# Optimization experiments

Measured on AMD Instinct MI355X. Metric: run time of the kernel, lower is better.

The kernel has to match this reference:

```python
import jax, jax.numpy as jnp
import numpy as np

EPS = 1e-5
B, T, D, H = 4096, 256, 36, 64


def setup_inputs() -> dict:
    key = jax.random.key(0)
    ks = jax.random.split(key, 24)
    f32 = jnp.float32
    u = lambda k, shape, s: jax.random.uniform(k, shape, f32, -s, s)
    sH = 1.0 / np.sqrt(H)   # GRUCell / Linear(in=64) init scale
    sD = 1.0 / np.sqrt(D)
    sC = 1.0 / np.sqrt(2 * D)  # combine Linear(72,36)
    return {
        "values": jax.random.normal(ks[0], (B, T, D), f32),
        "masks": (jax.random.uniform(ks[1], (B, T, D)) > 0.2).astype(f32),
        "deltas": jax.random.uniform(ks[2], (B, T, D), f32) * 5.0,
        "label": (jax.random.uniform(ks[3], (B,)) > 0.5).astype(f32),
        "is_train": jnp.ones((B,), f32),
        # GRUCell(108, 64): gate order r, z, n (PyTorch convention)
        "W_ih": u(ks[4], (3 * H, 3 * D), sH),
        "W_hh": u(ks[5], (3 * H, H), sH),
        "b_ih": u(ks[6], (3 * H,), sH),
        "b_hh": u(ks[7], (3 * H,), sH),
        "hist_W": u(ks[8], (1, H), sH),
        "hist_b": u(ks[9], (1,), sH),
        "feat_W": u(ks[10], (D, D), sD),
        "feat_b": u(ks[11], (D,), sD),
        "decay_W": u(ks[12], (D, D), sD),
        "decay_b": u(ks[13], (D,), sD),
        "comb_W": u(ks[14], (D, 2 * D), sC),
        "comb_b": u(ks[15], (D,), sC),
        "out_W": u(ks[16], (1, H), sH),
        "out_b": u(ks[17], (1,), sH),
    }


def reference(values, masks, deltas, label, is_train,
              W_ih, W_hh, b_ih, b_hh, hist_W, hist_b,
              feat_W, feat_b, decay_W, decay_b,
              comb_W, comb_b, out_W, out_b):
    feat_Wm = feat_W * (1.0 - jnp.eye(D, dtype=feat_W.dtype))  # zero diagonal

    def step(carry, xs):
        h, h_sum, il = carry
        value, mask, delta = xs  # each [B, D]
        msum = jnp.sum(mask) + EPS
        value_x = h @ hist_W.T + hist_b                      # [B, 1], broadcasts
        il = il + jnp.sum(jnp.abs(value_x - value) * mask) / msum
        value_c = mask * value + (1.0 - mask) * value_x
        gamma = jnp.exp(-jax.nn.relu(delta @ decay_W.T + decay_b))
        beta = jax.nn.sigmoid(jnp.concatenate([gamma, mask], axis=1) @ comb_W.T + comb_b)
        value_z = value_c @ feat_Wm.T + feat_b
        il = il + jnp.sum(jnp.abs(value_z - value) * mask) / msum
        value_h = value_z * beta + value_x * (1.0 - beta)
        il = il + jnp.sum(jnp.abs(value_h - value) * mask) / msum
        value_c = mask * value + (1.0 - mask) * value_h
        x = jnp.concatenate([value_c, mask, gamma], axis=1)  # [B, 3D]
        gi = x @ W_ih.T + b_ih
        gh = h @ W_hh.T + b_hh
        i_r, i_z, i_n = jnp.split(gi, 3, axis=1)
        h_r, h_z, h_n = jnp.split(gh, 3, axis=1)
        r = jax.nn.sigmoid(i_r + h_r)
        z = jax.nn.sigmoid(i_z + h_z)
        n = jnp.tanh(i_n + r * h_n)
        h_new = (1.0 - z) * n + z * h
        return (h_new, h_sum + h_new, il), value_c

    init = (jnp.zeros((B, H), values.dtype),
            jnp.zeros((B, H), values.dtype),
            jnp.zeros((), values.dtype))
    xs = (values.transpose(1, 0, 2), masks.transpose(1, 0, 2), deltas.transpose(1, 0, 2))
    (h, h_sum, impute_loss), imp = jax.lax.scan(step, init, xs)

    impute_loss = impute_loss / T
    h_sum = h_sum / T
    logits = h_sum @ out_W.T + out_b                          # [B, 1]
    y = label.reshape(-1, 1)
    w = is_train.reshape(-1, 1)
    # binary_cross_entropy_with_logits, reduce=False
    bce = jnp.maximum(logits, 0.0) - logits * y + jnp.log1p(jnp.exp(-jnp.abs(logits)))
    class_loss = jnp.sum(bce * w) / (jnp.sum(w) + EPS)
    loss = class_loss + impute_loss  # alpha = 1.0
    pred = jax.nn.sigmoid(logits)
    impute_values = imp.transpose(1, 0, 2).reshape(B, T * D)  # concat over time on dim 1
    return loss, impute_values, pred
```

## Files before the change

### kernel.cpp

```cpp
#include <hip/hip_runtime.h>
#include <hip/hip_bf16.h>


#define Bsz 4096
#define Tn  256
#define Dn  36
#define ROWS 16
#define EPSf 1e-5f
#define VMST 38

using f32x4 = __attribute__((ext_vector_type(4))) float;
using s8    = __attribute__((ext_vector_type(8))) short;

__device__ __forceinline__ short f2bf(float x) {
  return (short)__bfloat16_as_ushort(__float2bfloat16(x));
}
__device__ __forceinline__ float sigf(float x) { return 1.f / (1.f + __expf(-x)); }
__device__ __forceinline__ float tanhfast(float x) { return 1.f - 2.f / (1.f + __expf(2.f * x)); }
__device__ __forceinline__ int fragoff(int row, int k) {
  return ((k >> 5) << 9) + (((k >> 3) & 3) << 7) + (row << 3) + (k & 7);
}
__device__ __forceinline__ float selq(f32x4 v, int s) {
  float a = (s & 1) ? v[1] : v[0];
  float b = (s & 1) ? v[3] : v[2];
  return (s & 2) ? b : a;
}

__global__ void msum_k(const float4* __restrict__ masks4, float* __restrict__ rmsum) {
  int t = blockIdx.x;
  float s = 0.f;
  for (int r = threadIdx.x; r < Bsz; r += 256) {
    const float4* mp = masks4 + ((size_t)r * Tn + t) * 9;
    #pragma unroll
    for (int j = 0; j < 9; ++j) { float4 v = mp[j]; s += v.x + v.y + v.z + v.w; }
  }
  __shared__ float red[256];
  red[threadIdx.x] = s;
  __syncthreads();
  for (int k = 128; k > 0; k >>= 1) {
    if (threadIdx.x < k) red[threadIdx.x] += red[threadIdx.x + k];
    __syncthreads();
  }
  if (threadIdx.x == 0) rmsum[t] = 1.f / (red[0] + EPSf);
}

__global__ __launch_bounds__(512) void brits_main(
    const float* __restrict__ values, const float* __restrict__ masks,
    const float* __restrict__ deltas, const float* __restrict__ label,
    const float* __restrict__ is_train,
    const float* __restrict__ W_ih, const float* __restrict__ W_hh,
    const float* __restrict__ b_ih, const float* __restrict__ b_hh,
    const float* __restrict__ hist_W, const float* __restrict__ hist_b,
    const float* __restrict__ feat_W, const float* __restrict__ feat_b,
    const float* __restrict__ decay_W, const float* __restrict__ decay_b,
    const float* __restrict__ comb_W, const float* __restrict__ comb_b,
    const float* __restrict__ out_W, const float* __restrict__ out_b,
    float* __restrict__ out, const float* __restrict__ rmsum,
    float* __restrict__ ws_acc ) {

  __shared__ __align__(16) float2 vm_s[2][ROWS * VMST];
  __shared__ float  red_s[512];
  __shared__ float  red16[16];
  __shared__ __align__(16) short hbuf[1024];
  __shared__ __align__(16) short dbuf[2][1024];
  __shared__ __align__(16) short xbuf[2][2048];
  __shared__ __align__(16) short vcbuf[4][1024];
  __shared__ __align__(16) short cxbuf[4][1536];

  const int tid  = threadIdx.x;
  const int w    = tid >> 6;
  const int lane = tid & 63;
  const int lc   = lane & 15;
  const int r4   = lane >> 4;
  const int row0 = blockIdx.x * ROWS;
  const int k0b  = r4 * 8;
  const int lw8  = lane * 8;

  const bool isG = (w < 4);
  const int  sW  = isG ? 0 : (w - 4);
  const int  dim = 16 * (isG ? w : 0) + lc;
  const int  myrow = 4 * r4 + sW;

  s8 bf[23];
  #pragma unroll
  for (int i = 0; i < 23; ++i) bf[i] = (s8)(short)0;

  if (isG) {
    #pragma unroll
    for (int g = 0; g < 3; ++g) {
      const int n = 64 * g + dim;
      #pragma unroll
      for (int kt = 0; kt < 4; ++kt) {
        s8 f;
        #pragma unroll
        for (int e = 0; e < 8; ++e) {
          int xk = k0b + 32 * kt + e;
          float wv = 0.f;
          if (xk < 72) wv = W_ih[n * 108 + 36 + xk];
          else if (xk < 108) wv = W_ih[n * 108 + xk - 72];
          f[e] = f2bf(wv);
        }
        bf[g * 4 + kt] = f;
      }
      #pragma unroll
      for (int kt = 0; kt < 2; ++kt) {
        s8 f;
        #pragma unroll
        for (int e = 0; e < 8; ++e) f[e] = f2bf(W_hh[n * 64 + k0b + 32 * kt + e]);
        bf[12 + g * 2 + kt] = f;
      }
    }
  } else {
    #pragma unroll
    for (int t3 = 0; t3 < 3; ++t3) {
      const int col = 16 * t3 + lc;
      const bool cok = (col < Dn);
      #pragma unroll
      for (int kt = 0; kt < 2; ++kt) {
        s8 fd, ff;
        #pragma unroll
        for (int e = 0; e < 8; ++e) {
          int k = k0b + 32 * kt + e;
          fd[e] = f2bf((cok && k < Dn) ? decay_W[col * Dn + k] : 0.f);
          ff[e] = f2bf((cok && k < Dn && k != col) ? feat_W[col * Dn + k] : 0.f);
        }
        bf[t3 * 2 + kt] = fd;
        bf[6 + t3 * 2 + kt] = ff;
      }
      #pragma unroll
      for (int kt = 0; kt < 3; ++kt) {
        s8 f;
        #pragma unroll
        for (int e = 0; e < 8; ++e) {
          int k = k0b + 32 * kt + e;
          f[e] = f2bf((cok && k < 72) ? comb_W[col * 72 + k] : 0.f);
        }
        bf[12 + t3 * 3 + kt] = f;
      }
    }
    #pragma unroll
    for (int kt = 0; kt < 2; ++kt) {
      s8 f;
      #pragma unroll
      for (int e = 0; e < 8; ++e) f[e] = f2bf(hist_W[k0b + 32 * kt + e]);
      bf[21 + kt] = f;
    }
  }

  float db3[3] = {0,0,0}, fb3[3] = {0,0,0}, cb3[3] = {0,0,0};
  float br = 0.f, bz = 0.f, bin_ = 0.f, bhn = 0.f, ow = 0.f;
  if (isG) {
    br   = b_ih[dim] + b_hh[dim];
    bz   = b_ih[64 + dim] + b_hh[64 + dim];
    bin_ = b_ih[128 + dim];
    bhn  = b_hh[128 + dim];
    ow   = out_W[dim];
  } else {
    #pragma unroll
    for (int t3 = 0; t3 < 3; ++t3) {
      int col = 16 * t3 + lc;
      if (col < Dn) { db3[t3] = decay_b[col]; fb3[t3] = feat_b[col]; cb3[t3] = comb_b[col]; }
    }
  }
  const float histb = hist_b[0];
  const int hb = fragoff(0, dim);

  const bool stg = (tid < 144);
  const int srow = tid / 9;
  const int squad = tid - srow * 9;
  const size_t sbase = ((size_t)(row0 + srow) * Tn) * Dn + squad * 4;
  const int sfo = fragoff(srow, squad * 4);
  const int svo = srow * VMST + squad * 4;

  const int mrow = 4 * (lane / 9) + sW;
  const int mc0  = (lane % 9) * 4;

  for (int i = tid; i < 1024; i += 512) {
    hbuf[i] = 0; dbuf[0][i] = 0; dbuf[1][i] = 0;
    vcbuf[0][i] = 0; vcbuf[1][i] = 0; vcbuf[2][i] = 0; vcbuf[3][i] = 0;
  }
  for (int i = tid; i < 2048; i += 512) { xbuf[0][i] = 0; xbuf[1][i] = 0; }
  for (int i = tid; i < 1536; i += 512) {
    cxbuf[0][i] = 0; cxbuf[1][i] = 0; cxbuf[2][i] = 0; cxbuf[3][i] = 0;
  }
  __syncthreads();

  float4 pv = {0,0,0,0}, pm = {0,0,0,0}, pd = {0,0,0,0};
  if (stg) {
    float4 v0 = *(const float4*)&values[sbase];
    float4 m0 = *(const float4*)&masks[sbase];
    float4 d0 = *(const float4*)&deltas[sbase];
    *(float4*)&vm_s[0][svo]     = make_float4(v0.x, m0.x, v0.y, m0.y);
    *(float4*)&vm_s[0][svo + 2] = make_float4(v0.z, m0.z, v0.w, m0.w);
    union { short s[4]; uint2 u; } td, tm;
    td.s[0]=f2bf(d0.x); td.s[1]=f2bf(d0.y); td.s[2]=f2bf(d0.z); td.s[3]=f2bf(d0.w);
    tm.s[0]=f2bf(m0.x); tm.s[1]=f2bf(m0.y); tm.s[2]=f2bf(m0.z); tm.s[3]=f2bf(m0.w);
    *(uint2*)&dbuf[0][sfo] = td.u;
    *(uint2*)&xbuf[0][sfo] = tm.u;
    pv = *(const float4*)&values[sbase + Dn];
    pm = *(const float4*)&masks[sbase + Dn];
    pd = *(const float4*)&deltas[sbase + Dn];
  }
  __syncthreads();
  if (!isG && lane < 36) {
    #pragma unroll
    for (int j = 0; j < 4; ++j)
      cxbuf[sW][fragoff(mrow, 36 + mc0 + j)] = f2bf(vm_s[0][mrow * VMST + mc0 + j].y);
  }

  float hreg[4] = {0.f, 0.f, 0.f, 0.f};
  float lacc[4] = {0.f, 0.f, 0.f, 0.f};
  float il = 0.f;
  __syncthreads();

  #pragma unroll 1
  for (int t = 0; t < Tn; ++t) {
    const float srm = rmsum[t];
    const int p = t & 1;
    f32x4 A0 = {0,0,0,0}, A1 = {0,0,0,0}, A2 = {0,0,0,0}, A3 = {0,0,0,0};

    if (isG) {
      s8 ah0 = *(const s8*)&hbuf[lw8];
      s8 ah1 = *(const s8*)&hbuf[512 + lw8];
      s8 ax0 = *(const s8*)&xbuf[p][lw8];
      A0 = __builtin_amdgcn_mfma_f32_16x16x32_bf16(ah0, bf[12], A0, 0, 0, 0);
      A0 = __builtin_amdgcn_mfma_f32_16x16x32_bf16(ah1, bf[13], A0, 0, 0, 0);
      A1 = __builtin_amdgcn_mfma_f32_16x16x32_bf16(ah0, bf[14], A1, 0, 0, 0);
      A1 = __builtin_amdgcn_mfma_f32_16x16x32_bf16(ah1, bf[15], A1, 0, 0, 0);
      A3 = __builtin_amdgcn_mfma_f32_16x16x32_bf16(ah0, bf[16], A3, 0, 0, 0);
      A3 = __builtin_amdgcn_mfma_f32_16x16x32_bf16(ah1, bf[17], A3, 0, 0, 0);
      A0 = __builtin_amdgcn_mfma_f32_16x16x32_bf16(ax0, bf[0], A0, 0, 0, 0);
      A1 = __builtin_amdgcn_mfma_f32_16x16x32_bf16(ax0, bf[4], A1, 0, 0, 0);
      A2 = __builtin_amdgcn_mfma_f32_16x16x32_bf16(ax0, bf[8], A2, 0, 0, 0);
      if (stg && t + 1 < Tn) {
        *(float4*)&vm_s[p ^ 1][svo]     = make_float4(pv.x, pm.x, pv.y, pm.y);
        *(float4*)&vm_s[p ^ 1][svo + 2] = make_float4(pv.z, pm.z, pv.w, pm.w);
        union { short s[4]; uint2 u; } td, tm;
        td.s[0]=f2bf(pd.x); td.s[1]=f2bf(pd.y); td.s[2]=f2bf(pd.z); td.s[3]=f2bf(pd.w);
        tm.s[0]=f2bf(pm.x); tm.s[1]=f2bf(pm.y); tm.s[2]=f2bf(pm.z); tm.s[3]=f2bf(pm.w);
        *(uint2*)&dbuf[p ^ 1][sfo] = td.u;
        *(uint2*)&xbuf[p ^ 1][sfo] = tm.u;
      }
      if (stg && t + 2 < Tn) {
        size_t o = sbase + (size_t)(t + 2) * Dn;
        pv = *(const float4*)&values[o];
        pm = *(const float4*)&masks[o];
        pd = *(const float4*)&deltas[o];
      }
    } else {
      s8 ah0 = *(const s8*)&hbuf[lw8];
      s8 ah1 = *(const s8*)&hbuf[512 + lw8];
      s8 ad0 = *(const s8*)&dbuf[p][lw8];
      s8 ad1 = *(const s8*)&dbuf[p][512 + lw8];
      f32x4 X = {0,0,0,0};
      X = __builtin_amdgcn_mfma_f32_16x16x32_bf16(ah0, bf[21], X, 0, 0, 0);
      X = __builtin_amdgcn_mfma_f32_16x16x32_bf16(ah1, bf[22], X, 0, 0, 0);
      f32x4 Gm0 = {0,0,0,0}, Gm1 = {0,0,0,0}, Gm2 = {0,0,0,0};
      Gm0 = __builtin_amdgcn_mfma_f32_16x16x32_bf16(ad0, bf[0], Gm0, 0, 0, 0);
      Gm0 = __builtin_amdgcn_mfma_f32_16x16x32_bf16(ad1, bf[1], Gm0, 0, 0, 0);
      Gm1 = __builtin_amdgcn_mfma_f32_16x16x32_bf16(ad0, bf[2], Gm1, 0, 0, 0);
      Gm1 = __builtin_amdgcn_mfma_f32_16x16x32_bf16(ad1, bf[3], Gm1, 0, 0, 0);
      Gm2 = __builtin_amdgcn_mfma_f32_16x16x32_bf16(ad0, bf[4], Gm2, 0, 0, 0);
      Gm2 = __builtin_amdgcn_mfma_f32_16x16x32_bf16(ad1, bf[5], Gm2, 0, 0, 0);
      const float vx = selq(X, sW) + histb;

      float v3[3], m3[3];
      #pragma unroll
      for (int t3 = 0; t3 < 3; ++t3) {
        const int col = 16 * t3 + lc;
        float gmv = (t3 == 0) ? selq(Gm0, sW) : (t3 == 1) ? selq(Gm1, sW) : selq(Gm2, sW);
        v3[t3] = 0.f; m3[t3] = 0.f;
        if (col < Dn) {
          float g = __expf(-fmaxf(gmv + db3[t3], 0.f));
          short gbv = f2bf(g);
          xbuf[p][fragoff(myrow, 36 + col)] = gbv;
          cxbuf[sW][fragoff(myrow, col)]    = gbv;
          float2 vm = vm_s[p][myrow * VMST + col];
          v3[t3] = vm.x; m3[t3] = vm.y;
          il += srm * fabsf(vx - vm.x) * vm.y;
          vcbuf[sW][fragoff(myrow, col)] = f2bf(vm.y * vm.x + (1.f - vm.y) * vx);
        }
      }
      s8 av0 = *(const s8*)&vcbuf[sW][lw8];
      s8 av1 = *(const s8*)&vcbuf[sW][512 + lw8];
      f32x4 Z0 = {0,0,0,0}, Z1 = {0,0,0,0}, Z2 = {0,0,0,0};
      Z0 = __builtin_amdgcn_mfma_f32_16x16x32_bf16(av0, bf[6],  Z0, 0, 0, 0);
      Z0 = __builtin_amdgcn_mfma_f32_16x16x32_bf16(av1, bf[7],  Z0, 0, 0, 0);
      Z1 = __builtin_amdgcn_mfma_f32_16x16x32_bf16(av0, bf[8],  Z1, 0, 0, 0);
      Z1 = __builtin_amdgcn_mfma_f32_16x16x32_bf16(av1, bf[9],  Z1, 0, 0, 0);
      Z2 = __builtin_amdgcn_mfma_f32_16x16x32_bf16(av0, bf[10], Z2, 0, 0, 0);
      Z2 = __builtin_amdgcn_mfma_f32_16x16x32_bf16(av1, bf[11], Z2, 0, 0, 0);
      s8 ac0 = *(const s8*)&cxbuf[sW][lw8];
      s8 ac1 = *(const s8*)&cxbuf[sW][512 + lw8];
      s8 ac2 = *(const s8*)&cxbuf[sW][1024 + lw8];
      f32x4 B0 = {0,0,0,0}, B1 = {0,0,0,0}, B2 = {0,0,0,0};
      B0 = __builtin_amdgcn_mfma_f32_16x16x32_bf16(ac0, bf[12], B0, 0, 0, 0);
      B0 = __builtin_amdgcn_mfma_f32_16x16x32_bf16(ac1, bf[13], B0, 0, 0, 0);
      B0 = __builtin_amdgcn_mfma_f32_16x16x32_bf16(ac2, bf[14], B0, 0, 0, 0);
      B1 = __builtin_amdgcn_mfma_f32_16x16x32_bf16(ac0, bf[15], B1, 0, 0, 0);
      B1 = __builtin_amdgcn_mfma_f32_16x16x32_bf16(ac1, bf[16], B1, 0, 0, 0);
      B1 = __builtin_amdgcn_mfma_f32_16x16x32_bf16(ac2, bf[17], B1, 0, 0, 0);
      B2 = __builtin_amdgcn_mfma_f32_16x16x32_bf16(ac0, bf[18], B2, 0, 0, 0);
      B2 = __builtin_amdgcn_mfma_f32_16x16x32_bf16(ac1, bf[19], B2, 0, 0, 0);
      B2 = __builtin_amdgcn_mfma_f32_16x16x32_bf16(ac2, bf[20], B2, 0, 0, 0);
      #pragma unroll
      for (int t3 = 0; t3 < 3; ++t3) {
        const int col = 16 * t3 + lc;
        if (col < Dn) {
          float zv = (t3 == 0) ? selq(Z0, sW) : (t3 == 1) ? selq(Z1, sW) : selq(Z2, sW);
          float bv = (t3 == 0) ? selq(B0, sW) : (t3 == 1) ? selq(B1, sW) : selq(B2, sW);
          float beta = sigf(bv + cb3[t3]);
          float vz = zv + fb3[t3];
          il += srm * fabsf(vz - v3[t3]) * m3[t3];
          float vh = vz * beta + vx * (1.f - beta);
          il += srm * fabsf(vh - v3[t3]) * m3[t3];
          float vc2 = m3[t3] * v3[t3] + (1.f - m3[t3]) * vh;
          out[1 + ((size_t)(row0 + myrow) * Tn + t) * Dn + col] = vc2;
          xbuf[p][fragoff(myrow, 72 + col)] = f2bf(vc2);
        }
      }
    }
    __syncthreads();

    if (isG) {
      s8 ax1 = *(const s8*)&xbuf[p][512 + lw8];
      s8 ax2 = *(const s8*)&xbuf[p][1024 + lw8];
      s8 ax3 = *(const s8*)&xbuf[p][1536 + lw8];
      A0 = __builtin_amdgcn_mfma_f32_16x16x32_bf16(ax1, bf[1], A0, 0, 0, 0);
      A1 = __builtin_amdgcn_mfma_f32_16x16x32_bf16(ax1, bf[5], A1, 0, 0, 0);
      A2 = __builtin_amdgcn_mfma_f32_16x16x32_bf16(ax1, bf[9], A2, 0, 0, 0);
      A0 = __builtin_amdgcn_mfma_f32_16x16x32_bf16(ax2, bf[2], A0, 0, 0, 0);
      A1 = __builtin_amdgcn_mfma_f32_16x16x32_bf16(ax2, bf[6], A1, 0, 0, 0);
      A2 = __builtin_amdgcn_mfma_f32_16x16x32_bf16(ax2, bf[10], A2, 0, 0, 0);
      A0 = __builtin_amdgcn_mfma_f32_16x16x32_bf16(ax3, bf[3], A0, 0, 0, 0);
      A1 = __builtin_amdgcn_mfma_f32_16x16x32_bf16(ax3, bf[7], A1, 0, 0, 0);
      A2 = __builtin_amdgcn_mfma_f32_16x16x32_bf16(ax3, bf[11], A2, 0, 0, 0);
      #pragma unroll
      for (int q = 0; q < 4; ++q) {
        float rg = sigf(A0[q] + br);
        float zg = sigf(A1[q] + bz);
        float ng = tanhfast(A2[q] + bin_ + rg * (A3[q] + bhn));
        float hn = (1.f - zg) * ng + zg * hreg[q];
        hreg[q] = hn;
        lacc[q] += hn * ow;
        hbuf[hb + (r4 * 4 + q) * 8] = f2bf(hn);
      }
    } else {
      if (t + 1 < Tn && lane < 36) {
        #pragma unroll
        for (int j = 0; j < 4; ++j)
          cxbuf[sW][fragoff(mrow, 36 + mc0 + j)] =
              f2bf(vm_s[p ^ 1][mrow * VMST + mc0 + j].y);
      }
    }
    __syncthreads();
  }

  red_s[tid] = il;
  __syncthreads();
  for (int k = 256; k > 0; k >>= 1) {
    if (tid < k) red_s[tid] += red_s[tid + k];
    __syncthreads();
  }
  if (tid == 0) atomicAdd(&ws_acc[0], red_s[0]);
  if (tid < 16) red16[tid] = 0.f;
  __syncthreads();
  if (isG) {
    #pragma unroll
    for (int q = 0; q < 4; ++q) atomicAdd(&red16[r4 * 4 + q], lacc[q]);
  }
  __syncthreads();

  if (tid < ROWS) {
    float lg = red16[tid] / (float)Tn + out_b[0];
    int rg = row0 + tid;
    float pred = sigf(lg);
    out[1 + (size_t)Bsz * Tn * Dn + rg] = pred;
    float y = label[rg], wt = is_train[rg];
    float bce = fmaxf(lg, 0.f) - lg * y + log1pf(__expf(-fabsf(lg)));
    atomicAdd(&ws_acc[1], bce * wt);
    atomicAdd(&ws_acc[2], wt);
  }
}

__global__ void fin_k(const float* __restrict__ ws, float* __restrict__ out) {
  out[0] = ws[1] / (ws[2] + EPSf) + ws[0] / (float)Tn;
}

extern "C" void kernel_launch(void* const* d_in, const int* in_sizes, int n_in,
                              void* d_out, int out_size, void* d_ws, size_t ws_size,
                              hipStream_t stream) {
  const float* values   = (const float*)d_in[0];
  const float* masks    = (const float*)d_in[1];
  const float* deltas   = (const float*)d_in[2];
  const float* label    = (const float*)d_in[3];
  const float* is_train = (const float*)d_in[4];
  const float* W_ih     = (const float*)d_in[5];
  const float* W_hh     = (const float*)d_in[6];
  const float* b_ih     = (const float*)d_in[7];
  const float* b_hh     = (const float*)d_in[8];
  const float* hist_W   = (const float*)d_in[9];
  const float* hist_b   = (const float*)d_in[10];
  const float* feat_W   = (const float*)d_in[11];
  const float* feat_b   = (const float*)d_in[12];
  const float* decay_W  = (const float*)d_in[13];
  const float* decay_b  = (const float*)d_in[14];
  const float* comb_W   = (const float*)d_in[15];
  const float* comb_b   = (const float*)d_in[16];
  const float* out_W    = (const float*)d_in[17];
  const float* out_b    = (const float*)d_in[18];

  float* ws = (float*)d_ws;
  float* rmsum = ws + 4;
  float* out = (float*)d_out;

  hipMemsetAsync(d_ws, 0, 16, stream);
  msum_k<<<Tn, 256, 0, stream>>>((const float4*)masks, rmsum);
  brits_main<<<Bsz / ROWS, 512, 0, stream>>>(
      values, masks, deltas, label, is_train, W_ih, W_hh, b_ih, b_hh,
      hist_W, hist_b, feat_W, feat_b, decay_W, decay_b, comb_W, comb_b,
      out_W, out_b, out, rmsum, ws);
  fin_k<<<1, 1, 0, stream>>>(ws, out);
}
```

Measured before the change: 447.6 us.

## Precompute next-step decay/beta in phase two and move weights to LDS

The decay (gamma) and combine (beta) matmuls for step t+1 move into the second phase of step t, which was mostly idle for the side waves. This shortens the critical first phase that gates the GRU update. W_hh and comb_W fragments now live in shared memory rather than registers, cutting register use so launch_bounds(512,4) can be requested. The cost is more LDS traffic and a larger LDS footprint, which may itself limit occupancy.

```diff
diff --git a/kernel.cpp b/kernel.cpp
--- a/kernel.cpp
+++ b/kernel.cpp
@@ -25,6 +25,7 @@
   float b = (s & 1) ? v[3] : v[2];
   return (s & 2) ? b : a;
 }
+#define MFMA __builtin_amdgcn_mfma_f32_16x16x32_bf16
 
 __global__ void msum_k(const float4* __restrict__ masks4, float* __restrict__ rmsum) {
   int t = blockIdx.x;
@@ -44,7 +45,7 @@
   if (threadIdx.x == 0) rmsum[t] = 1.f / (red[0] + EPSf);
 }
 
-__global__ __launch_bounds__(512) void brits_main(
+__global__ __launch_bounds__(512, 4) void brits_main(
     const float* __restrict__ values, const float* __restrict__ masks,
     const float* __restrict__ deltas, const float* __restrict__ label,
     const float* __restrict__ is_train,
@@ -59,13 +60,14 @@
     float* __restrict__ ws_acc ) {
 
   __shared__ __align__(16) float2 vm_s[2][ROWS * VMST];
-  __shared__ float  red_s[512];
-  __shared__ float  red16[16];
   __shared__ __align__(16) short hbuf[1024];
   __shared__ __align__(16) short dbuf[2][1024];
   __shared__ __align__(16) short xbuf[2][2048];
   __shared__ __align__(16) short vcbuf[4][1024];
   __shared__ __align__(16) short cxbuf[4][1536];
+  __shared__ __align__(16) short whh_l[24 * 512];
+  __shared__ __align__(16) short comb_l[9 * 512];
+  __shared__ float red16[16];
 
   const int tid  = threadIdx.x;
   const int w    = tid >> 6;
@@ -81,9 +83,9 @@
   const int  dim = 16 * (isG ? w : 0) + lc;
   const int  myrow = 4 * r4 + sW;
 
-  s8 bf[23];
+  s8 bf[14];
   #pragma unroll
-  for (int i = 0; i < 23; ++i) bf[i] = (s8)(short)0;
+  for (int i = 0; i < 14; ++i) bf[i] = (s8)(short)0;
 
   if (isG) {
     #pragma unroll
@@ -107,7 +109,7 @@
         s8 f;
         #pragma unroll
         for (int e = 0; e < 8; ++e) f[e] = f2bf(W_hh[n * 64 + k0b + 32 * kt + e]);
-        bf[12 + g * 2 + kt] = f;
+        *(s8*)&whh_l[(w * 6 + g * 2 + kt) * 512 + lw8] = f;
       }
     }
   } else {
@@ -127,23 +129,30 @@
         bf[t3 * 2 + kt] = fd;
         bf[6 + t3 * 2 + kt] = ff;
       }
-      #pragma unroll
-      for (int kt = 0; kt < 3; ++kt) {
-        s8 f;
-        #pragma unroll
-        for (int e = 0; e < 8; ++e) {
-          int k = k0b + 32 * kt + e;
-          f[e] = f2bf((cok && k < 72) ? comb_W[col * 72 + k] : 0.f);
-        }
-        bf[12 + t3 * 3 + kt] = f;
-      }
     }
     #pragma unroll
     for (int kt = 0; kt < 2; ++kt) {
       s8 f;
       #pragma unroll
       for (int e = 0; e < 8; ++e) f[e] = f2bf(hist_W[k0b + 32 * kt + e]);
-      bf[21 + kt] = f;
+      bf[12 + kt] = f;
+    }
+    if (w == 4) {
+      #pragma unroll
+      for (int t3 = 0; t3 < 3; ++t3) {
+        const int col = 16 * t3 + lc;
+        const bool cok = (col < Dn);
+        #pragma unroll
+        for (int kt = 0; kt < 3; ++kt) {
+          s8 f;
+          #pragma unroll
+          for (int e = 0; e < 8; ++e) {
+            int k = k0b + 32 * kt + e;
+            f[e] = f2bf((cok && k < 72) ? comb_W[col * 72 + k] : 0.f);
+          }
+          *(s8*)&comb_l[(t3 * 3 + kt) * 512 + lw8] = f;
+        }
+      }
     }
   }
 
@@ -202,10 +211,46 @@
     pd = *(const float4*)&deltas[sbase + Dn];
   }
   __syncthreads();
-  if (!isG && lane < 36) {
-    #pragma unroll
-    for (int j = 0; j < 4; ++j)
-      cxbuf[sW][fragoff(mrow, 36 + mc0 + j)] = f2bf(vm_s[0][mrow * VMST + mc0 + j].y);
+
+  float bq[3] = {0.f, 0.f, 0.f};
+  if (!isG) {
+    s8 ad0 = *(const s8*)&dbuf[0][lw8];
+    s8 ad1 = *(const s8*)&dbuf[0][512 + lw8];
+    f32x4 G0 = {0,0,0,0}, G1 = {0,0,0,0}, G2 = {0,0,0,0};
+    G0 = MFMA(ad0, bf[0], G0, 0,0,0); G0 = MFMA(ad1, bf[1], G0, 0,0,0);
+    G1 = MFMA(ad0, bf[2], G1, 0,0,0); G1 = MFMA(ad1, bf[3], G1, 0,0,0);
+    G2 = MFMA(ad0, bf[4], G2, 0,0,0); G2 = MFMA(ad1, bf[5], G2, 0,0,0);
+    #pragma unroll
+    for (int t3 = 0; t3 < 3; ++t3) {
+      int col = 16 * t3 + lc;
+      if (col < Dn) {
+        float gm = (t3==0) ? selq(G0,sW) : (t3==1) ? selq(G1,sW) : selq(G2,sW);
+        short gbv = f2bf(__expf(-fmaxf(gm + db3[t3], 0.f)));
+        xbuf[0][fragoff(myrow, 36 + col)] = gbv;
+        cxbuf[sW][fragoff(myrow, col)] = gbv;
+      }
+    }
+    if (lane < 36) {
+      #pragma unroll
+      for (int j = 0; j < 4; ++j)
+        cxbuf[sW][fragoff(mrow, 36 + mc0 + j)] = f2bf(vm_s[0][mrow * VMST + mc0 + j].y);
+    }
+    s8 ac0 = *(const s8*)&cxbuf[sW][lw8];
+    s8 ac1 = *(const s8*)&cxbuf[sW][512 + lw8];
+    s8 ac2 = *(const s8*)&cxbuf[sW][1024 + lw8];
+    f32x4 B0 = {0,0,0,0}, B1 = {0,0,0,0}, B2 = {0,0,0,0};
+    B0 = MFMA(ac0, *(const s8*)&comb_l[0*512+lw8], B0, 0,0,0);
+    B0 = MFMA(ac1, *(const s8*)&comb_l[1*512+lw8], B0, 0,0,0);
+    B0 = MFMA(ac2, *(const s8*)&comb_l[2*512+lw8], B0, 0,0,0);
+    B1 = MFMA(ac0, *(const s8*)&comb_l[3*512+lw8], B1, 0,0,0);
+    B1 = MFMA(ac1, *(const s8*)&comb_l[4*512+lw8], B1, 0,0,0);
+    B1 = MFMA(ac2, *(const s8*)&comb_l[5*512+lw8], B1, 0,0,0);
+    B2 = MFMA(ac0, *(const s8*)&comb_l[6*512+lw8], B2, 0,0,0);
+    B2 = MFMA(ac1, *(const s8*)&comb_l[7*512+lw8], B2, 0,0,0);
+    B2 = MFMA(ac2, *(const s8*)&comb_l[8*512+lw8], B2, 0,0,0);
+    bq[0] = sigf(selq(B0,sW) + cb3[0]);
+    bq[1] = sigf(selq(B1,sW) + cb3[1]);
+    bq[2] = sigf(selq(B2,sW) + cb3[2]);
   }
 
   float hreg[4] = {0.f, 0.f, 0.f, 0.f};
@@ -220,18 +265,20 @@
     f32x4 A0 = {0,0,0,0}, A1 = {0,0,0,0}, A2 = {0,0,0,0}, A3 = {0,0,0,0};
 
     if (isG) {
+      const int wb = w * 6 * 512;
       s8 ah0 = *(const s8*)&hbuf[lw8];
       s8 ah1 = *(const s8*)&hbuf[512 + lw8];
+      A0 = MFMA(ah0, *(const s8*)&whh_l[wb + lw8],        A0, 0,0,0);
+      A0 = MFMA(ah1, *(const s8*)&whh_l[wb + 512 + lw8],  A0, 0,0,0);
+      A1 = MFMA(ah0, *(const s8*)&whh_l[wb + 1024 + lw8], A1, 0,0,0);
+      A1 = MFMA(ah1, *(const s8*)&whh_l[wb + 1536 + lw8], A1, 0,0,0);
+      A3 = MFMA(ah0, *(const s8*)&whh_l[wb + 2048 + lw8], A3, 0,0,0);
+      A3 = MFMA(ah1, *(const s8*)&whh_l[wb + 2560 + lw8], A3, 0,0,0);
       s8 ax0 = *(const s8*)&xbuf[p][lw8];
-      A0 = __builtin_amdgcn_mfma_f32_16x16x32_bf16(ah0, bf[12], A0, 0, 0, 0);
-      A0 = __builtin_amdgcn_mfma_f32_16x16x32_bf16(ah1, bf[13], A0, 0, 0, 0);
-      A1 = __builtin_amdgcn_mfma_f32_16x16x32_bf16(ah0, bf[14], A1, 0, 0, 0);
-      A1 = __builtin_amdgcn_mfma_f32_16x16x32_bf16(ah1, bf[15], A1, 0, 0, 0);
-      A3 = __builtin_amdgcn_mfma_f32_16x16x32_bf16(ah0, bf[16], A3, 0, 0, 0);
-      A3 = __builtin_amdgcn_mfma_f32_16x16x32_bf16(ah1, bf[17], A3, 0, 0, 0);
-      A0 = __builtin_amdgcn_mfma_f32_16x16x32_bf16(ax0, bf[0], A0, 0, 0, 0);
-      A1 = __builtin_amdgcn_mfma_f32_16x16x32_bf16(ax0, bf[4], A1, 0, 0, 0);
-      A2 = __builtin_amdgcn_mfma_f32_16x16x32_bf16(ax0, bf[8], A2, 0, 0, 0);
+      s8 ax1 = *(const s8*)&xbuf[p][512 + lw8];
+      A0 = MFMA(ax0, bf[0], A0, 0,0,0); A0 = MFMA(ax1, bf[1], A0, 0,0,0);
+      A1 = MFMA(ax0, bf[4], A1, 0,0,0); A1 = MFMA(ax1, bf[5], A1, 0,0,0);
+      A2 = MFMA(ax0, bf[8], A2, 0,0,0); A2 = MFMA(ax1, bf[9], A2, 0,0,0);
       if (stg && t + 1 < Tn) {
         *(float4*)&vm_s[p ^ 1][svo]     = make_float4(pv.x, pm.x, pv.y, pm.y);
         *(float4*)&vm_s[p ^ 1][svo + 2] = make_float4(pv.z, pm.z, pv.w, pm.w);
@@ -250,31 +297,16 @@
     } else {
       s8 ah0 = *(const s8*)&hbuf[lw8];
       s8 ah1 = *(const s8*)&hbuf[512 + lw8];
-      s8 ad0 = *(const s8*)&dbuf[p][lw8];
-      s8 ad1 = *(const s8*)&dbuf[p][512 + lw8];
       f32x4 X = {0,0,0,0};
-      X = __builtin_amdgcn_mfma_f32_16x16x32_bf16(ah0, bf[21], X, 0, 0, 0);
-      X = __builtin_amdgcn_mfma_f32_16x16x32_bf16(ah1, bf[22], X, 0, 0, 0);
-      f32x4 Gm0 = {0,0,0,0}, Gm1 = {0,0,0,0}, Gm2 = {0,0,0,0};
-      Gm0 = __builtin_amdgcn_mfma_f32_16x16x32_bf16(ad0, bf[0], Gm0, 0, 0, 0);
-      Gm0 = __builtin_amdgcn_mfma_f32_16x16x32_bf16(ad1, bf[1], Gm0, 0, 0, 0);
-      Gm1 = __builtin_amdgcn_mfma_f32_16x16x32_bf16(ad0, bf[2], Gm1, 0, 0, 0);
-      Gm1 = __builtin_amdgcn_mfma_f32_16x16x32_bf16(ad1, bf[3], Gm1, 0, 0, 0);
-      Gm2 = __builtin_amdgcn_mfma_f32_16x16x32_bf16(ad0, bf[4], Gm2, 0, 0, 0);
-      Gm2 = __builtin_amdgcn_mfma_f32_16x16x32_bf16(ad1, bf[5], Gm2, 0, 0, 0);
+      X = MFMA(ah0, bf[12], X, 0,0,0);
+      X = MFMA(ah1, bf[13], X, 0,0,0);
       const float vx = selq(X, sW) + histb;
-
       float v3[3], m3[3];
       #pragma unroll
       for (int t3 = 0; t3 < 3; ++t3) {
-        const int col = 16 * t3 + lc;
-        float gmv = (t3 == 0) ? selq(Gm0, sW) : (t3 == 1) ? selq(Gm1, sW) : selq(Gm2, sW);
+        int col = 16 * t3 + lc;
         v3[t3] = 0.f; m3[t3] = 0.f;
         if (col < Dn) {
-          float g = __expf(-fmaxf(gmv + db3[t3], 0.f));
-          short gbv = f2bf(g);
-          xbuf[p][fragoff(myrow, 36 + col)] = gbv;
-          cxbuf[sW][fragoff(myrow, col)]    = gbv;
           float2 vm = vm_s[p][myrow * VMST + col];
           v3[t3] = vm.x; m3[t3] = vm.y;
           il += srm * fabsf(vx - vm.x) * vm.y;
@@ -284,35 +316,16 @@
       s8 av0 = *(const s8*)&vcbuf[sW][lw8];
       s8 av1 = *(const s8*)&vcbuf[sW][512 + lw8];
       f32x4 Z0 = {0,0,0,0}, Z1 = {0,0,0,0}, Z2 = {0,0,0,0};
-      Z0 = __builtin_amdgcn_mfma_f32_16x16x32_bf16(av0, bf[6],  Z0, 0, 0, 0);
-      Z0 = __builtin_amdgcn_mfma_f32_16x16x32_bf16(av1, bf[7],  Z0, 0, 0, 0);
-      Z1 = __builtin_amdgcn_mfma_f32_16x16x32_bf16(av0, bf[8],  Z1, 0, 0, 0);
-      Z1 = __builtin_amdgcn_mfma_f32_16x16x32_bf16(av1, bf[9],  Z1, 0, 0, 0);
-      Z2 = __builtin_amdgcn_mfma_f32_16x16x32_bf16(av0, bf[10], Z2, 0, 0, 0);
-      Z2 = __builtin_amdgcn_mfma_f32_16x16x32_bf16(av1, bf[11], Z2, 0, 0, 0);
-      s8 ac0 = *(const s8*)&cxbuf[sW][lw8];
-      s8 ac1 = *(const s8*)&cxbuf[sW][512 + lw8];
-      s8 ac2 = *(const s8*)&cxbuf[sW][1024 + lw8];
-      f32x4 B0 = {0,0,0,0}, B1 = {0,0,0,0}, B2 = {0,0,0,0};
-      B0 = __builtin_amdgcn_mfma_f32_16x16x32_bf16(ac0, bf[12], B0, 0, 0, 0);
-      B0 = __builtin_amdgcn_mfma_f32_16x16x32_bf16(ac1, bf[13], B0, 0, 0, 0);
-      B0 = __builtin_amdgcn_mfma_f32_16x16x32_bf16(ac2, bf[14], B0, 0, 0, 0);
-      B1 = __builtin_amdgcn_mfma_f32_16x16x32_bf16(ac0, bf[15], B1, 0, 0, 0);
-      B1 = __builtin_amdgcn_mfma_f32_16x16x32_bf16(ac1, bf[16], B1, 0, 0, 0);
-      B1 = __builtin_amdgcn_mfma_f32_16x16x32_bf16(ac2, bf[17], B1, 0, 0, 0);
-      B2 = __builtin_amdgcn_mfma_f32_16x16x32_bf16(ac0, bf[18], B2, 0, 0, 0);
-      B2 = __builtin_amdgcn_mfma_f32_16x16x32_bf16(ac1, bf[19], B2, 0, 0, 0);
-      B2 = __builtin_amdgcn_mfma_f32_16x16x32_bf16(ac2, bf[20], B2, 0, 0, 0);
+      Z0 = MFMA(av0, bf[6],  Z0, 0,0,0); Z0 = MFMA(av1, bf[7],  Z0, 0,0,0);
+      Z1 = MFMA(av0, bf[8],  Z1, 0,0,0); Z1 = MFMA(av1, bf[9],  Z1, 0,0,0);
+      Z2 = MFMA(av0, bf[10], Z2, 0,0,0); Z2 = MFMA(av1, bf[11], Z2, 0,0,0);
       #pragma unroll
       for (int t3 = 0; t3 < 3; ++t3) {
-        const int col = 16 * t3 + lc;
+        int col = 16 * t3 + lc;
         if (col < Dn) {
-          float zv = (t3 == 0) ? selq(Z0, sW) : (t3 == 1) ? selq(Z1, sW) : selq(Z2, sW);
-          float bv = (t3 == 0) ? selq(B0, sW) : (t3 == 1) ? selq(B1, sW) : selq(B2, sW);
-          float beta = sigf(bv + cb3[t3]);
-          float vz = zv + fb3[t3];
+          float vz = ((t3==0) ? selq(Z0,sW) : (t3==1) ? selq(Z1,sW) : selq(Z2,sW)) + fb3[t3];
           il += srm * fabsf(vz - v3[t3]) * m3[t3];
-          float vh = vz * beta + vx * (1.f - beta);
+          float vh = vz * bq[t3] + vx * (1.f - bq[t3]);
           il += srm * fabsf(vh - v3[t3]) * m3[t3];
           float vc2 = m3[t3] * v3[t3] + (1.f - m3[t3]) * vh;
           out[1 + ((size_t)(row0 + myrow) * Tn + t) * Dn + col] = vc2;
@@ -323,18 +336,11 @@
     __syncthreads();
 
     if (isG) {
-      s8 ax1 = *(const s8*)&xbuf[p][512 + lw8];
       s8 ax2 = *(const s8*)&xbuf[p][1024 + lw8];
       s8 ax3 = *(const s8*)&xbuf[p][1536 + lw8];
-      A0 = __builtin_amdgcn_mfma_f32_16x16x32_bf16(ax1, bf[1], A0, 0, 0, 0);
-      A1 = __builtin_amdgcn_mfma_f32_16x16x32_bf16(ax1, bf[5], A1, 0, 0, 0);
-      A2 = __builtin_amdgcn_mfma_f32_16x16x32_bf16(ax1, bf[9], A2, 0, 0, 0);
-      A0 = __builtin_amdgcn_mfma_f32_16x16x32_bf16(ax2, bf[2], A0, 0, 0, 0);
-      A1 = __builtin_amdgcn_mfma_f32_16x16x32_bf16(ax2, bf[6], A1, 0, 0, 0);
-      A2 = __builtin_amdgcn_mfma_f32_16x16x32_bf16(ax2, bf[10], A2, 0, 0, 0);
-      A0 = __builtin_amdgcn_mfma_f32_16x16x32_bf16(ax3, bf[3], A0, 0, 0, 0);
-      A1 = __builtin_amdgcn_mfma_f32_16x16x32_bf16(ax3, bf[7], A1, 0, 0, 0);
-      A2 = __builtin_amdgcn_mfma_f32_16x16x32_bf16(ax3, bf[11], A2, 0, 0, 0);
+      A0 = MFMA(ax2, bf[2],  A0, 0,0,0); A0 = MFMA(ax3, bf[3],  A0, 0,0,0);
+      A1 = MFMA(ax2, bf[6],  A1, 0,0,0); A1 = MFMA(ax3, bf[7],  A1, 0,0,0);
+      A2 = MFMA(ax2, bf[10], A2, 0,0,0); A2 = MFMA(ax3, bf[11], A2, 0,0,0);
       #pragma unroll
       for (int q = 0; q < 4; ++q) {
         float rg = sigf(A0[q] + br);
@@ -345,17 +351,50 @@
         lacc[q] += hn * ow;
         hbuf[hb + (r4 * 4 + q) * 8] = f2bf(hn);
       }
-    } else {
-      if (t + 1 < Tn && lane < 36) {
+    } else if (t + 1 < Tn) {
+      s8 ad0 = *(const s8*)&dbuf[p ^ 1][lw8];
+      s8 ad1 = *(const s8*)&dbuf[p ^ 1][512 + lw8];
+      f32x4 G0 = {0,0,0,0}, G1 = {0,0,0,0}, G2 = {0,0,0,0};
+      G0 = MFMA(ad0, bf[0], G0, 0,0,0); G0 = MFMA(ad1, bf[1], G0, 0,0,0);
+      G1 = MFMA(ad0, bf[2], G1, 0,0,0); G1 = MFMA(ad1, bf[3], G1, 0,0,0);
+      G2 = MFMA(ad0, bf[4], G2, 0,0,0); G2 = MFMA(ad1, bf[5], G2, 0,0,0);
+      #pragma unroll
+      for (int t3 = 0; t3 < 3; ++t3) {
+        int col = 16 * t3 + lc;
+        if (col < Dn) {
+          float gm = (t3==0) ? selq(G0,sW) : (t3==1) ? selq(G1,sW) : selq(G2,sW);
+          short gbv = f2bf(__expf(-fmaxf(gm + db3[t3], 0.f)));
+          xbuf[p ^ 1][fragoff(myrow, 36 + col)] = gbv;
+          cxbuf[sW][fragoff(myrow, col)] = gbv;
+        }
+      }
+      if (lane < 36) {
         #pragma unroll
         for (int j = 0; j < 4; ++j)
           cxbuf[sW][fragoff(mrow, 36 + mc0 + j)] =
               f2bf(vm_s[p ^ 1][mrow * VMST + mc0 + j].y);
       }
+      s8 ac0 = *(const s8*)&cxbuf[sW][lw8];
+      s8 ac1 = *(const s8*)&cxbuf[sW][512 + lw8];
+      s8 ac2 = *(const s8*)&cxbuf[sW][1024 + lw8];
+      f32x4 B0 = {0,0,0,0}, B1 = {0,0,0,0}, B2 = {0,0,0,0};
+      B0 = MFMA(ac0, *(const s8*)&comb_l[0*512+lw8], B0, 0,0,0);
+      B0 = MFMA(ac1, *(const s8*)&comb_l[1*512+lw8], B0, 0,0,0);
+      B0 = MFMA(ac2, *(const s8*)&comb_l[2*512+lw8], B0, 0,0,0);
+      B1 = MFMA(ac0, *(const s8*)&comb_l[3*512+lw8], B1, 0,0,0);
+      B1 = MFMA(ac1, *(const s8*)&comb_l[4*512+lw8], B1, 0,0,0);
+      B1 = MFMA(ac2, *(const s8*)&comb_l[5*512+lw8], B1, 0,0,0);
+      B2 = MFMA(ac0, *(const s8*)&comb_l[6*512+lw8], B2, 0,0,0);
+      B2 = MFMA(ac1, *(const s8*)&comb_l[7*512+lw8], B2, 0,0,0);
+      B2 = MFMA(ac2, *(const s8*)&comb_l[8*512+lw8], B2, 0,0,0);
+      bq[0] = sigf(selq(B0,sW) + cb3[0]);
+      bq[1] = sigf(selq(B1,sW) + cb3[1]);
+      bq[2] = sigf(selq(B2,sW) + cb3[2]);
     }
     __syncthreads();
   }
 
+  float* red_s = (float*)whh_l;
   red_s[tid] = il;
   __syncthreads();
   for (int k = 256; k > 0; k >>= 1) {
```

Result: slower. 1.173 ms (+161.9%).
